# Performance work log

Hardware: AMD Instinct MI355X
Metric: run time of the kernel (lower is better)

The kernel has to match this reference:

```python
import jax, jax.numpy as jnp
import numpy as np

B, H, S, D = 2, 16, 2048, 64

def setup_inputs() -> dict:
    key = jax.random.key(0)
    kq, kk, kv, km = jax.random.split(key, 4)
    Q = jax.random.normal(kq, (B, H, S, D), dtype=jnp.float32)
    K = jax.random.normal(kk, (B, H, S, D), dtype=jnp.float32)
    V = jax.random.normal(kv, (B, H, S, D), dtype=jnp.float32)
    # padding-style boolean mask, broadcast over heads; True = masked out
    attn_mask = jax.random.randint(km, (B, 1, S, S), 0, 2).astype(jnp.bool_)
    return {"Q": Q, "K": K, "V": V, "attn_mask": attn_mask}

def reference(Q, K, V, attn_mask):
    d = Q.shape[-1]
    scale = 1.0 / np.sqrt(d).astype(np.float32)
    # [B,H,S,S] scores
    scores = jnp.einsum('bhqd,bhkd->bhqk', Q, K) * scale
    scores = jnp.where(attn_mask, jnp.float32(-1e9), scores)
    attn = jax.nn.softmax(scores, axis=-1)
    context = jnp.einsum('bhqk,bhkd->bhqd', attn, V)
    return context
```

## Files before the change

kernel.cpp:

```cpp
#include <hip/hip_runtime.h>

#define B_ 2
#define H_ 16
#define S_ 2048
#define D_ 64
#define BK 32
#define NKT (S_ / BK)
#define ZSPLIT 2
#define NKT_Z (NKT / ZSPLIT)
#define QSCALE 0.18033688011112042f
#define MFIX 16.0f

#define KSD 36
#define VTD 18
#define KS_SZ (BK * KSD)
#define VT_SZ (D_ * VTD)

#define BHSD ((size_t)B_ * H_ * S_ * D_)
#define BHS  ((size_t)B_ * H_ * S_)

typedef __attribute__((ext_vector_type(4))) float  float4v;
typedef __attribute__((ext_vector_type(2))) _Float16 half2v;
typedef __attribute__((ext_vector_type(4))) _Float16 half4v;
typedef __attribute__((ext_vector_type(8))) _Float16 half8v;
typedef __attribute__((ext_vector_type(2))) __fp16 fp16x2;
typedef __attribute__((ext_vector_type(2))) unsigned uint2v;

union H2U { half2v h; fp16x2 g; unsigned u; };
union H4U { half4v h4; half2v h2[2]; fp16x2 g2[2]; uint2v u2; };
union H8U { half8v h8; fp16x2 g2[4]; };

__device__ __forceinline__ unsigned pkh(float a, float b) {
    H2U c; c.g = __builtin_amdgcn_cvt_pkrtz(a, b);
    return c.u;
}
__device__ __forceinline__ float fexp2(float x) {
#if __has_builtin(__builtin_amdgcn_exp2f)
    return __builtin_amdgcn_exp2f(x);
#else
    return exp2f(x);
#endif
}

__device__ __forceinline__ void wg_barrier() {
    asm volatile("s_waitcnt lgkmcnt(0)\n\ts_barrier" ::: "memory");
}

struct Stage { float4 k0, k1, va, vb; };

__device__ __forceinline__ void stage_load(const float* __restrict__ Kg,
                                           const float* __restrict__ Vg,
                                           int kk, int dd, Stage& s) {
    s.k0 = *(const float4*)(Kg + (size_t)kk * D_ + dd);
    s.k1 = *(const float4*)(Kg + (size_t)(kk + 16) * D_ + dd);
    s.va = *(const float4*)(Vg + (size_t)(2 * kk) * D_ + dd);
    s.vb = *(const float4*)(Vg + (size_t)(2 * kk + 1) * D_ + dd);
}

__device__ __forceinline__ void stage_store(unsigned* KsB, unsigned* VtB,
                                            int kwa, int kwb, const int* vw,
                                            const Stage& s) {
    *(uint2v*)&KsB[kwa] = (uint2v){ pkh(s.k0.x, s.k0.y), pkh(s.k0.z, s.k0.w) };
    *(uint2v*)&KsB[kwb] = (uint2v){ pkh(s.k1.x, s.k1.y), pkh(s.k1.z, s.k1.w) };
    VtB[vw[0]] = pkh(s.va.x, s.vb.x);
    VtB[vw[1]] = pkh(s.va.y, s.vb.y);
    VtB[vw[2]] = pkh(s.va.z, s.vb.z);
    VtB[vw[3]] = pkh(s.va.w, s.vb.w);
}

__device__ __forceinline__ float4 mask2bias(int4 m) {
    float4 r;
    r.x = m.x ? -1e9f : -MFIX;  r.y = m.y ? -1e9f : -MFIX;
    r.z = m.z ? -1e9f : -MFIX;  r.w = m.w ? -1e9f : -MFIX;
    return r;
}

__global__ __launch_bounds__(256, 4)
void attn_flash_sk(const float* __restrict__ Q, const float* __restrict__ K,
                   const float* __restrict__ V, const int* __restrict__ mask,
                   float* __restrict__ Opart, float* __restrict__ Lpart)
{
    __shared__ unsigned KsAll[2 * KS_SZ];
    __shared__ unsigned VtAll[2 * VT_SZ];

    const int tid  = threadIdx.x;
    const int lane = tid & 63;
    const int l15  = lane & 15;
    const int quad = lane >> 4;
    const int wave = tid >> 6;
    const int bh   = blockIdx.y;
    const int b    = bh / H_;
    const int qbase = blockIdx.x * 64 + wave * 16;
    const size_t qkv = (size_t)bh * S_ * D_;

    const int ktBegin = blockIdx.z * NKT_Z;
    const int ktEnd   = ktBegin + NKT_Z;

    half8v qf[2];
    {
        const float* qrow = Q + qkv + (size_t)(qbase + l15) * D_ + quad * 8;
        #pragma unroll
        for (int dc = 0; dc < 2; ++dc) {
            float4 f0 = *(const float4*)(qrow + dc * 32);
            float4 f1 = *(const float4*)(qrow + dc * 32 + 4);
            H8U u;
            u.g2[0] = __builtin_amdgcn_cvt_pkrtz(f0.x * QSCALE, f0.y * QSCALE);
            u.g2[1] = __builtin_amdgcn_cvt_pkrtz(f0.z * QSCALE, f0.w * QSCALE);
            u.g2[2] = __builtin_amdgcn_cvt_pkrtz(f1.x * QSCALE, f1.y * QSCALE);
            u.g2[3] = __builtin_amdgcn_cvt_pkrtz(f1.z * QSCALE, f1.w * QSCALE);
            qf[dc] = u.h8;
        }
    }

    const int kk = tid >> 4;
    const int dd = (tid & 15) * 4;
    const int kwa = kk * KSD + (tid & 15) * 2;
    const int kwb = (kk + 16) * KSD + (tid & 15) * 2;
    int vw[4];
    #pragma unroll
    for (int m = 0; m < 4; ++m)
        vw[m] = (dd + m) * VTD + (kk ^ ((((dd + m) >> 4) & 3) << 1));

    int kroff[2][2];
    #pragma unroll
    for (int t = 0; t < 2; ++t)
        #pragma unroll
        for (int dc = 0; dc < 2; ++dc)
            kroff[t][dc] = (t * 16 + l15) * KSD + dc * 16 + quad * 4;
    int vrd[4][2];
    #pragma unroll
    for (int nb = 0; nb < 4; ++nb)
        #pragma unroll
        for (int t = 0; t < 2; ++t)
            vrd[nb][t] = (nb * 16 + l15) * VTD + ((t * 8 + quad * 2) ^ ((nb & 3) << 1));

    const int* mrow0 = mask + (size_t)b * S_ * S_ + (size_t)(qbase + l15) * S_ + quad * 4;

    float l_lane = 0.0f;
    float4v o[4];
    #pragma unroll
    for (int nb = 0; nb < 4; ++nb) o[nb] = (float4v){0.f, 0.f, 0.f, 0.f};

    const float* Kg0 = K + qkv;
    const float* Vg0 = V + qkv;

    Stage sA, sB;
    stage_load(Kg0 + (size_t)ktBegin * BK * D_, Vg0 + (size_t)ktBegin * BK * D_, kk, dd, sA);
    stage_store(KsAll, VtAll, kwa, kwb, vw, sA);
    stage_load(Kg0 + (size_t)(ktBegin + 1) * BK * D_, Vg0 + (size_t)(ktBegin + 1) * BK * D_, kk, dd, sB);
    float4 mk0 = mask2bias(*(const int4*)(mrow0 + (size_t)ktBegin * BK));
    float4 mk1 = mask2bias(*(const int4*)(mrow0 + (size_t)ktBegin * BK + 16));
    wg_barrier();

    auto iter = [&](int kt, const unsigned* KsB, const unsigned* VtB,
                    unsigned* KsN, unsigned* VtN, Stage& pre, Stage& sto) {
        const int ktn = (kt + 2 < ktEnd) ? kt + 2 : ktEnd - 1;
        stage_load(Kg0 + (size_t)ktn * BK * D_, Vg0 + (size_t)ktn * BK * D_, kk, dd, pre);
        const int mtn = (kt + 1 < ktEnd) ? kt + 1 : ktEnd - 1;
        const int* mnext = mrow0 + (size_t)mtn * BK;
        const float4 nm0 = mask2bias(*(const int4*)(mnext));
        const float4 nm1 = mask2bias(*(const int4*)(mnext + 16));

        float4v st0 = (float4v){0.f,0.f,0.f,0.f}, st1 = st0;
        {
            half8v kf;
            kf = *(const half8v*)&KsB[kroff[0][0]];
            st0 = __builtin_amdgcn_mfma_f32_16x16x32_f16(kf, qf[0], st0, 0, 0, 0);
            kf = *(const half8v*)&KsB[kroff[0][1]];
            st0 = __builtin_amdgcn_mfma_f32_16x16x32_f16(kf, qf[1], st0, 0, 0, 0);
            kf = *(const half8v*)&KsB[kroff[1][0]];
            st1 = __builtin_amdgcn_mfma_f32_16x16x32_f16(kf, qf[0], st1, 0, 0, 0);
            kf = *(const half8v*)&KsB[kroff[1][1]];
            st1 = __builtin_amdgcn_mfma_f32_16x16x32_f16(kf, qf[1], st1, 0, 0, 0);
        }

        float4v p0, p1;
        p0.x = fexp2(st0.x + mk0.x); p0.y = fexp2(st0.y + mk0.y);
        p0.z = fexp2(st0.z + mk0.z); p0.w = fexp2(st0.w + mk0.w);
        p1.x = fexp2(st1.x + mk1.x); p1.y = fexp2(st1.y + mk1.y);
        p1.z = fexp2(st1.z + mk1.z); p1.w = fexp2(st1.w + mk1.w);

        l_lane += ((p0.x + p0.y) + (p0.z + p0.w)) +
                  ((p1.x + p1.y) + (p1.z + p1.w));

        H4U pf0u, pf1u;
        pf0u.g2[0] = __builtin_amdgcn_cvt_pkrtz(p0.x, p0.y);
        pf0u.g2[1] = __builtin_amdgcn_cvt_pkrtz(p0.z, p0.w);
        pf1u.g2[0] = __builtin_amdgcn_cvt_pkrtz(p1.x, p1.y);
        pf1u.g2[1] = __builtin_amdgcn_cvt_pkrtz(p1.z, p1.w);

        #pragma unroll
        for (int nb = 0; nb < 4; ++nb) {
            H4U vf;
            vf.u2 = *(const uint2v*)&VtB[vrd[nb][0]];
            o[nb] = __builtin_amdgcn_mfma_f32_16x16x16f16(vf.h4, pf0u.h4, o[nb], 0, 0, 0);
            vf.u2 = *(const uint2v*)&VtB[vrd[nb][1]];
            o[nb] = __builtin_amdgcn_mfma_f32_16x16x16f16(vf.h4, pf1u.h4, o[nb], 0, 0, 0);
        }

        stage_store(KsN, VtN, kwa, kwb, vw, sto);
        wg_barrier();
        mk0 = nm0; mk1 = nm1;
    };

    #pragma unroll 1
    for (int kt2 = ktBegin; kt2 < ktEnd; kt2 += 2) {
        iter(kt2,     KsAll,         VtAll,         (unsigned*)KsAll + KS_SZ, (unsigned*)VtAll + VT_SZ, sA, sB);
        iter(kt2 + 1, KsAll + KS_SZ, VtAll + VT_SZ, (unsigned*)KsAll,         (unsigned*)VtAll,         sB, sA);
    }

    float ls = l_lane;
    ls += __shfl_xor(ls, 16, 64);
    ls += __shfl_xor(ls, 32, 64);

    float* orow = Opart + (size_t)blockIdx.z * BHSD + qkv
                  + (size_t)(qbase + l15) * D_ + quad * 4;
    #pragma unroll
    for (int nb = 0; nb < 4; ++nb) {
        float4 ov = { o[nb].x, o[nb].y, o[nb].z, o[nb].w };
        *(float4*)(orow + nb * 16) = ov;
    }
    if (quad == 0)
        Lpart[(size_t)blockIdx.z * BHS + (size_t)bh * S_ + qbase + l15] = ls;
}

__global__ __launch_bounds__(256)
void attn_combine(const float* __restrict__ Opart, const float* __restrict__ Lpart,
                  float* __restrict__ out)
{
    const size_t i = (size_t)blockIdx.x * 256 + threadIdx.x;
    const size_t row = i >> 4;
    const float l = Lpart[row] + Lpart[BHS + row];
    const float inv = 1.0f / l;
    const float4 a = ((const float4*)Opart)[i];
    const float4 c = ((const float4*)Opart)[BHSD / 4 + i];
    float4 r = { (a.x + c.x) * inv, (a.y + c.y) * inv,
                 (a.z + c.z) * inv, (a.w + c.w) * inv };
    ((float4*)out)[i] = r;
}

__global__ __launch_bounds__(256, 4)
void attn_flash_st(const float* __restrict__ Q, const float* __restrict__ K,
                   const float* __restrict__ V, const int* __restrict__ mask,
                   float* __restrict__ out)
{
    __shared__ unsigned KsAll[2 * KS_SZ];
    __shared__ unsigned VtAll[2 * VT_SZ];

    const int tid  = threadIdx.x;
    const int lane = tid & 63;
    const int l15  = lane & 15;
    const int quad = lane >> 4;
    const int wave = tid >> 6;
    const int bh   = blockIdx.y;
    const int b    = bh / H_;
    const int qbase = blockIdx.x * 64 + wave * 16;
    const size_t qkv = (size_t)bh * S_ * D_;

    half8v qf[2];
    {
        const float* qrow = Q + qkv + (size_t)(qbase + l15) * D_ + quad * 8;
        #pragma unroll
        for (int dc = 0; dc < 2; ++dc) {
            float4 f0 = *(const float4*)(qrow + dc * 32);
            float4 f1 = *(const float4*)(qrow + dc * 32 + 4);
            H8U u;
            u.g2[0] = __builtin_amdgcn_cvt_pkrtz(f0.x * QSCALE, f0.y * QSCALE);
            u.g2[1] = __builtin_amdgcn_cvt_pkrtz(f0.z * QSCALE, f0.w * QSCALE);
            u.g2[2] = __builtin_amdgcn_cvt_pkrtz(f1.x * QSCALE, f1.y * QSCALE);
            u.g2[3] = __builtin_amdgcn_cvt_pkrtz(f1.z * QSCALE, f1.w * QSCALE);
            qf[dc] = u.h8;
        }
    }

    const int kk = tid >> 4;
    const int dd = (tid & 15) * 4;
    const int kwa = kk * KSD + (tid & 15) * 2;
    const int kwb = (kk + 16) * KSD + (tid & 15) * 2;
    int vw[4];
    #pragma unroll
    for (int m = 0; m < 4; ++m)
        vw[m] = (dd + m) * VTD + (kk ^ ((((dd + m) >> 4) & 3) << 1));

    int kroff[2][2];
    #pragma unroll
    for (int t = 0; t < 2; ++t)
        #pragma unroll
        for (int dc = 0; dc < 2; ++dc)
            kroff[t][dc] = (t * 16 + l15) * KSD + dc * 16 + quad * 4;
    int vrd[4][2];
    #pragma unroll
    for (int nb = 0; nb < 4; ++nb)
        #pragma unroll
        for (int t = 0; t < 2; ++t)
            vrd[nb][t] = (nb * 16 + l15) * VTD + ((t * 8 + quad * 2) ^ ((nb & 3) << 1));

    const int* mrow0 = mask + (size_t)b * S_ * S_ + (size_t)(qbase + l15) * S_ + quad * 4;

    float l_lane = 0.0f;
    float4v o[4];
    #pragma unroll
    for (int nb = 0; nb < 4; ++nb) o[nb] = (float4v){0.f, 0.f, 0.f, 0.f};

    const float* Kg0 = K + qkv;
    const float* Vg0 = V + qkv;

    Stage sA, sB;
    stage_load(Kg0, Vg0, kk, dd, sA);
    stage_store(KsAll, VtAll, kwa, kwb, vw, sA);
    stage_load(Kg0 + BK * D_, Vg0 + BK * D_, kk, dd, sB);
    float4 mk0 = mask2bias(*(const int4*)(mrow0));
    float4 mk1 = mask2bias(*(const int4*)(mrow0 + 16));
    wg_barrier();

    auto iter = [&](int kt, const unsigned* KsB, const unsigned* VtB,
                    unsigned* KsN, unsigned* VtN, Stage& pre, Stage& sto) {
        const int ktn = (kt + 2 < NKT) ? kt + 2 : NKT - 1;
        stage_load(Kg0 + (size_t)ktn * BK * D_, Vg0 + (size_t)ktn * BK * D_, kk, dd, pre);
        const int mtn = (kt + 1 < NKT) ? kt + 1 : NKT - 1;
        const int* mnext = mrow0 + (size_t)mtn * BK;
        const float4 nm0 = mask2bias(*(const int4*)(mnext));
        const float4 nm1 = mask2bias(*(const int4*)(mnext + 16));

        float4v st0 = (float4v){0.f,0.f,0.f,0.f}, st1 = st0;
        {
            half8v kf;
            kf = *(const half8v*)&KsB[kroff[0][0]];
            st0 = __builtin_amdgcn_mfma_f32_16x16x32_f16(kf, qf[0], st0, 0, 0, 0);
            kf = *(const half8v*)&KsB[kroff[0][1]];
            st0 = __builtin_amdgcn_mfma_f32_16x16x32_f16(kf, qf[1], st0, 0, 0, 0);
            kf = *(const half8v*)&KsB[kroff[1][0]];
            st1 = __builtin_amdgcn_mfma_f32_16x16x32_f16(kf, qf[0], st1, 0, 0, 0);
            kf = *(const half8v*)&KsB[kroff[1][1]];
            st1 = __builtin_amdgcn_mfma_f32_16x16x32_f16(kf, qf[1], st1, 0, 0, 0);
        }

        float4v p0, p1;
        p0.x = fexp2(st0.x + mk0.x); p0.y = fexp2(st0.y + mk0.y);
        p0.z = fexp2(st0.z + mk0.z); p0.w = fexp2(st0.w + mk0.w);
        p1.x = fexp2(st1.x + mk1.x); p1.y = fexp2(st1.y + mk1.y);
        p1.z = fexp2(st1.z + mk1.z); p1.w = fexp2(st1.w + mk1.w);

        l_lane += ((p0.x + p0.y) + (p0.z + p0.w)) +
                  ((p1.x + p1.y) + (p1.z + p1.w));

        H4U pf0u, pf1u;
        pf0u.g2[0] = __builtin_amdgcn_cvt_pkrtz(p0.x, p0.y);
        pf0u.g2[1] = __builtin_amdgcn_cvt_pkrtz(p0.z, p0.w);
        pf1u.g2[0] = __builtin_amdgcn_cvt_pkrtz(p1.x, p1.y);
        pf1u.g2[1] = __builtin_amdgcn_cvt_pkrtz(p1.z, p1.w);

        #pragma unroll
        for (int nb = 0; nb < 4; ++nb) {
            H4U vf;
            vf.u2 = *(const uint2v*)&VtB[vrd[nb][0]];
            o[nb] = __builtin_amdgcn_mfma_f32_16x16x16f16(vf.h4, pf0u.h4, o[nb], 0, 0, 0);
            vf.u2 = *(const uint2v*)&VtB[vrd[nb][1]];
            o[nb] = __builtin_amdgcn_mfma_f32_16x16x16f16(vf.h4, pf1u.h4, o[nb], 0, 0, 0);
        }

        stage_store(KsN, VtN, kwa, kwb, vw, sto);
        wg_barrier();
        mk0 = nm0; mk1 = nm1;
    };

    #pragma unroll 1
    for (int kt2 = 0; kt2 < NKT; kt2 += 2) {
        iter(kt2,     KsAll,         VtAll,         (unsigned*)KsAll + KS_SZ, (unsigned*)VtAll + VT_SZ, sA, sB);
        iter(kt2 + 1, KsAll + KS_SZ, VtAll + VT_SZ, (unsigned*)KsAll,         (unsigned*)VtAll,         sB, sA);
    }

    float ls = l_lane;
    ls += __shfl_xor(ls, 16, 64);
    ls += __shfl_xor(ls, 32, 64);
    const float inv = 1.0f / ls;

    float* orow = out + qkv + (size_t)(qbase + l15) * D_ + quad * 4;
    #pragma unroll
    for (int nb = 0; nb < 4; ++nb) {
        float4 ov = { o[nb].x * inv, o[nb].y * inv, o[nb].z * inv, o[nb].w * inv };
        *(float4*)(orow + nb * 16) = ov;
    }
}

extern "C" void kernel_launch(void* const* d_in, const int* in_sizes, int n_in,
                              void* d_out, int out_size, void* d_ws, size_t ws_size,
                              hipStream_t stream) {
    const float* Q    = (const float*)d_in[0];
    const float* K    = (const float*)d_in[1];
    const float* V    = (const float*)d_in[2];
    const int*   mask = (const int*)d_in[3];
    float* out = (float*)d_out;

    const size_t opBytes = BHSD * ZSPLIT * sizeof(float);
    const size_t lpBytes = BHS  * ZSPLIT * sizeof(float);
    const size_t needFull = opBytes + lpBytes;

    if (d_ws && ws_size >= needFull) {
        float* Opart = (float*)d_ws;
        float* Lpart = (float*)((char*)d_ws + opBytes);
        attn_flash_sk<<<dim3(S_ / 64, B_ * H_, ZSPLIT), dim3(256), 0, stream>>>(
            Q, K, V, mask, Opart, Lpart);
        attn_combine<<<dim3((unsigned)(BHSD / 4 / 256)), dim3(256), 0, stream>>>(
            Opart, Lpart, out);
    } else {
        attn_flash_st<<<dim3(S_ / 64, B_ * H_), dim3(256), 0, stream>>>(
            Q, K, V, mask, out);
    }
}
```

Measured before the change: 220.2 us.

## Pre-pack K/V into fp16 LDS-image tiles via separate kernel before attention

Adds a pack_kv kernel that converts K and V to fp16 once and writes them in the exact padded and swizzled shared-memory layout, including the transposed V. The attention kernel then just copies whole tile images from global memory into LDS with vector loads, instead of each of the 32 query blocks per head redoing fp32 loads, conversion and transposed scattered stores. This removes redundant conversion work and halves K/V read bytes in the main kernel. In exchange it adds an extra launch and a global write/read of the image, and raises the occupancy hint to 6.

```diff
diff --git a/kernel.cpp b/kernel.cpp
--- a/kernel.cpp
+++ b/kernel.cpp
@@ -6,18 +6,17 @@
 #define D_ 64
 #define BK 32
 #define NKT (S_ / BK)
-#define ZSPLIT 2
-#define NKT_Z (NKT / ZSPLIT)
 #define QSCALE 0.18033688011112042f
 #define MFIX 16.0f
 
 #define KSD 36
 #define VTD 18
-#define KS_SZ (BK * KSD)
-#define VT_SZ (D_ * VTD)
+#define TILE_DW 2304
+#define TILE_BYTES 9216
 
 #define BHSD ((size_t)B_ * H_ * S_ * D_)
 #define BHS  ((size_t)B_ * H_ * S_)
+#define IMG_DW ((size_t)B_ * H_ * NKT * TILE_DW)
 
 typedef __attribute__((ext_vector_type(4))) float  float4v;
 typedef __attribute__((ext_vector_type(2))) _Float16 half2v;
@@ -25,6 +24,7 @@
 typedef __attribute__((ext_vector_type(8))) _Float16 half8v;
 typedef __attribute__((ext_vector_type(2))) __fp16 fp16x2;
 typedef __attribute__((ext_vector_type(2))) unsigned uint2v;
+typedef __attribute__((ext_vector_type(4))) unsigned uint4v;
 
 union H2U { half2v h; fp16x2 g; unsigned u; };
 union H4U { half4v h4; half2v h2[2]; fp16x2 g2[2]; uint2v u2; };
@@ -46,42 +46,49 @@
     asm volatile("s_waitcnt lgkmcnt(0)\n\ts_barrier" ::: "memory");
 }
 
-struct Stage { float4 k0, k1, va, vb; };
-
-__device__ __forceinline__ void stage_load(const float* __restrict__ Kg,
-                                           const float* __restrict__ Vg,
-                                           int kk, int dd, Stage& s) {
-    s.k0 = *(const float4*)(Kg + (size_t)kk * D_ + dd);
-    s.k1 = *(const float4*)(Kg + (size_t)(kk + 16) * D_ + dd);
-    s.va = *(const float4*)(Vg + (size_t)(2 * kk) * D_ + dd);
-    s.vb = *(const float4*)(Vg + (size_t)(2 * kk + 1) * D_ + dd);
-}
-
-__device__ __forceinline__ void stage_store(unsigned* KsB, unsigned* VtB,
-                                            int kwa, int kwb, const int* vw,
-                                            const Stage& s) {
-    *(uint2v*)&KsB[kwa] = (uint2v){ pkh(s.k0.x, s.k0.y), pkh(s.k0.z, s.k0.w) };
-    *(uint2v*)&KsB[kwb] = (uint2v){ pkh(s.k1.x, s.k1.y), pkh(s.k1.z, s.k1.w) };
-    VtB[vw[0]] = pkh(s.va.x, s.vb.x);
-    VtB[vw[1]] = pkh(s.va.y, s.vb.y);
-    VtB[vw[2]] = pkh(s.va.z, s.vb.z);
-    VtB[vw[3]] = pkh(s.va.w, s.vb.w);
-}
-
-__device__ __forceinline__ float4 mask2bias(int4 m) {
-    float4 r;
-    r.x = m.x ? -1e9f : -MFIX;  r.y = m.y ? -1e9f : -MFIX;
-    r.z = m.z ? -1e9f : -MFIX;  r.w = m.w ? -1e9f : -MFIX;
-    return r;
-}
-
-__global__ __launch_bounds__(256, 4)
-void attn_flash_sk(const float* __restrict__ Q, const float* __restrict__ K,
-                   const float* __restrict__ V, const int* __restrict__ mask,
-                   float* __restrict__ Opart, float* __restrict__ Lpart)
+__global__ __launch_bounds__(256)
+void pack_kv(const float* __restrict__ K, const float* __restrict__ V,
+             unsigned* __restrict__ img)
 {
-    __shared__ unsigned KsAll[2 * KS_SZ];
-    __shared__ unsigned VtAll[2 * VT_SZ];
+    __shared__ float Kf[32 * 64];
+    __shared__ float Vf[32 * 64];
+    const int tid = threadIdx.x;
+    const int kt = blockIdx.x, bh = blockIdx.y;
+    const size_t base = ((size_t)bh * S_ + (size_t)kt * 32) * D_;
+
+    const int rr = tid >> 4, c4 = (tid & 15) * 4;
+    *(float4*)&Kf[rr * 64 + c4]        = *(const float4*)(K + base + (size_t)rr * D_ + c4);
+    *(float4*)&Kf[(rr + 16) * 64 + c4] = *(const float4*)(K + base + (size_t)(rr + 16) * D_ + c4);
+    *(float4*)&Vf[rr * 64 + c4]        = *(const float4*)(V + base + (size_t)rr * D_ + c4);
+    *(float4*)&Vf[(rr + 16) * 64 + c4] = *(const float4*)(V + base + (size_t)(rr + 16) * D_ + c4);
+    __syncthreads();
+
+    unsigned* out = img + (size_t)(bh * NKT + kt) * TILE_DW;
+    #pragma unroll
+    for (int p = 0; p < 9; ++p) {
+        const int P = p * 256 + tid;
+        unsigned val = 0u;
+        if (P < 1152) {
+            const int r2 = P / 36, pd = P % 36;
+            if (pd < 32) val = pkh(Kf[r2 * 64 + 2 * pd], Kf[r2 * 64 + 2 * pd + 1]);
+        } else {
+            const int Pv = P - 1152;
+            const int r = Pv / 18, c = Pv % 18;
+            if (c < 16) {
+                const int ct = c ^ ((((r >> 4) & 3) << 1));
+                val = pkh(Vf[(2 * ct) * 64 + r], Vf[(2 * ct + 1) * 64 + r]);
+            }
+        }
+        out[P] = val;
+    }
+}
+
+__global__ __launch_bounds__(256, 6)
+void attn_img(const float* __restrict__ Q, const unsigned* __restrict__ img,
+              const int* __restrict__ mask, float* __restrict__ out,
+              float* __restrict__ Opart, float* __restrict__ Lpart)
+{
+    __shared__ unsigned Buf[2 * TILE_DW];
 
     const int tid  = threadIdx.x;
     const int lane = tid & 63;
@@ -93,8 +100,10 @@
     const int qbase = blockIdx.x * 64 + wave * 16;
     const size_t qkv = (size_t)bh * S_ * D_;
 
-    const int ktBegin = blockIdx.z * NKT_Z;
-    const int ktEnd   = ktBegin + NKT_Z;
+    const int zsplit = gridDim.z;
+    const int nkt    = NKT / zsplit;
+    const int ktB    = blockIdx.z * nkt;
+    const int ktE    = ktB + nkt;
 
     half8v qf[2];
     {
@@ -112,116 +121,126 @@
         }
     }
 
-    const int kk = tid >> 4;
-    const int dd = (tid & 15) * 4;
-    const int kwa = kk * KSD + (tid & 15) * 2;
-    const int kwb = (kk + 16) * KSD + (tid & 15) * 2;
-    int vw[4];
-    #pragma unroll
-    for (int m = 0; m < 4; ++m)
-        vw[m] = (dd + m) * VTD + (kk ^ ((((dd + m) >> 4) & 3) << 1));
-
-    int kroff[2][2];
-    #pragma unroll
-    for (int t = 0; t < 2; ++t)
-        #pragma unroll
-        for (int dc = 0; dc < 2; ++dc)
-            kroff[t][dc] = (t * 16 + l15) * KSD + dc * 16 + quad * 4;
-    int vrd[4][2];
+    const int kbase = l15 * KSD + quad * 4;
+    int vrd4[4];
     #pragma unroll
     for (int nb = 0; nb < 4; ++nb)
-        #pragma unroll
-        for (int t = 0; t < 2; ++t)
-            vrd[nb][t] = (nb * 16 + l15) * VTD + ((t * 8 + quad * 2) ^ ((nb & 3) << 1));
+        vrd4[nb] = 1152 + nb * 16 * VTD + l15 * VTD + ((quad * 2) ^ ((nb & 3) << 1));
 
     const int* mrow0 = mask + (size_t)b * S_ * S_ + (size_t)(qbase + l15) * S_ + quad * 4;
+
+    const unsigned* gsrc = img + (size_t)(bh * NKT + ktB) * TILE_DW;
+    const int wa = 4 * tid;
+    uint4v sa, sb; unsigned sc;
 
     float l_lane = 0.0f;
     float4v o[4];
     #pragma unroll
     for (int nb = 0; nb < 4; ++nb) o[nb] = (float4v){0.f, 0.f, 0.f, 0.f};
 
-    const float* Kg0 = K + qkv;
-    const float* Vg0 = V + qkv;
-
-    Stage sA, sB;
-    stage_load(Kg0 + (size_t)ktBegin * BK * D_, Vg0 + (size_t)ktBegin * BK * D_, kk, dd, sA);
-    stage_store(KsAll, VtAll, kwa, kwb, vw, sA);
-    stage_load(Kg0 + (size_t)(ktBegin + 1) * BK * D_, Vg0 + (size_t)(ktBegin + 1) * BK * D_, kk, dd, sB);
-    float4 mk0 = mask2bias(*(const int4*)(mrow0 + (size_t)ktBegin * BK));
-    float4 mk1 = mask2bias(*(const int4*)(mrow0 + (size_t)ktBegin * BK + 16));
+    sa = *(const uint4v*)(gsrc + wa);
+    sb = *(const uint4v*)(gsrc + 1024 + wa);
+    sc = gsrc[2048 + tid];
+    *(uint4v*)&Buf[wa]        = sa;
+    *(uint4v*)&Buf[1024 + wa] = sb;
+    Buf[2048 + tid]           = sc;
+    gsrc += TILE_DW;
+    sa = *(const uint4v*)(gsrc + wa);
+    sb = *(const uint4v*)(gsrc + 1024 + wa);
+    sc = gsrc[2048 + tid];
+    int4 mA0 = *(const int4*)(mrow0 + (size_t)ktB * BK);
+    int4 mA1 = *(const int4*)(mrow0 + (size_t)ktB * BK + 16);
+    int4 mB0, mB1;
     wg_barrier();
 
-    auto iter = [&](int kt, const unsigned* KsB, const unsigned* VtB,
-                    unsigned* KsN, unsigned* VtN, Stage& pre, Stage& sto) {
-        const int ktn = (kt + 2 < ktEnd) ? kt + 2 : ktEnd - 1;
-        stage_load(Kg0 + (size_t)ktn * BK * D_, Vg0 + (size_t)ktn * BK * D_, kk, dd, pre);
-        const int mtn = (kt + 1 < ktEnd) ? kt + 1 : ktEnd - 1;
-        const int* mnext = mrow0 + (size_t)mtn * BK;
-        const float4 nm0 = mask2bias(*(const int4*)(mnext));
-        const float4 nm1 = mask2bias(*(const int4*)(mnext + 16));
+    auto body = [&](int kt, const unsigned* cur, unsigned* oth,
+                    const int4 c0, const int4 c1, int4& n0, int4& n1) {
+        *(uint4v*)&oth[wa]        = sa;
+        *(uint4v*)&oth[1024 + wa] = sb;
+        oth[2048 + tid]           = sc;
+        if (kt + 2 < ktE) gsrc += TILE_DW;
+        sa = *(const uint4v*)(gsrc + wa);
+        sb = *(const uint4v*)(gsrc + 1024 + wa);
+        sc = gsrc[2048 + tid];
 
         float4v st0 = (float4v){0.f,0.f,0.f,0.f}, st1 = st0;
         {
             half8v kf;
-            kf = *(const half8v*)&KsB[kroff[0][0]];
+            kf = *(const half8v*)&cur[kbase];
             st0 = __builtin_amdgcn_mfma_f32_16x16x32_f16(kf, qf[0], st0, 0, 0, 0);
-            kf = *(const half8v*)&KsB[kroff[0][1]];
+            kf = *(const half8v*)&cur[kbase + 16];
             st0 = __builtin_amdgcn_mfma_f32_16x16x32_f16(kf, qf[1], st0, 0, 0, 0);
-            kf = *(const half8v*)&KsB[kroff[1][0]];
+            kf = *(const half8v*)&cur[kbase + 576];
             st1 = __builtin_amdgcn_mfma_f32_16x16x32_f16(kf, qf[0], st1, 0, 0, 0);
-            kf = *(const half8v*)&KsB[kroff[1][1]];
+            kf = *(const half8v*)&cur[kbase + 576 + 16];
             st1 = __builtin_amdgcn_mfma_f32_16x16x32_f16(kf, qf[1], st1, 0, 0, 0);
         }
 
+        const int mtn = (kt + 1 < ktE) ? kt + 1 : ktE - 1;
+        n0 = *(const int4*)(mrow0 + (size_t)mtn * BK);
+        n1 = *(const int4*)(mrow0 + (size_t)mtn * BK + 16);
+
         float4v p0, p1;
-        p0.x = fexp2(st0.x + mk0.x); p0.y = fexp2(st0.y + mk0.y);
-        p0.z = fexp2(st0.z + mk0.z); p0.w = fexp2(st0.w + mk0.w);
-        p1.x = fexp2(st1.x + mk1.x); p1.y = fexp2(st1.y + mk1.y);
-        p1.z = fexp2(st1.z + mk1.z); p1.w = fexp2(st1.w + mk1.w);
+        p0.x = fexp2(st0.x + (c0.x ? -1e9f : -MFIX));
+        p0.y = fexp2(st0.y + (c0.y ? -1e9f : -MFIX));
+        p0.z = fexp2(st0.z + (c0.z ? -1e9f : -MFIX));
+        p0.w = fexp2(st0.w + (c0.w ? -1e9f : -MFIX));
+        p1.x = fexp2(st1.x + (c1.x ? -1e9f : -MFIX));
+        p1.y = fexp2(st1.y + (c1.y ? -1e9f : -MFIX));
+        p1.z = fexp2(st1.z + (c1.z ? -1e9f : -MFIX));
+        p1.w = fexp2(st1.w + (c1.w ? -1e9f : -MFIX));
 
         l_lane += ((p0.x + p0.y) + (p0.z + p0.w)) +
                   ((p1.x + p1.y) + (p1.z + p1.w));
 
-        H4U pf0u, pf1u;
-        pf0u.g2[0] = __builtin_amdgcn_cvt_pkrtz(p0.x, p0.y);
-        pf0u.g2[1] = __builtin_amdgcn_cvt_pkrtz(p0.z, p0.w);
-        pf1u.g2[0] = __builtin_amdgcn_cvt_pkrtz(p1.x, p1.y);
-        pf1u.g2[1] = __builtin_amdgcn_cvt_pkrtz(p1.z, p1.w);
+        H4U pf0, pf1;
+        pf0.g2[0] = __builtin_amdgcn_cvt_pkrtz(p0.x, p0.y);
+        pf0.g2[1] = __builtin_amdgcn_cvt_pkrtz(p0.z, p0.w);
+        pf1.g2[0] = __builtin_amdgcn_cvt_pkrtz(p1.x, p1.y);
+        pf1.g2[1] = __builtin_amdgcn_cvt_pkrtz(p1.z, p1.w);
 
         #pragma unroll
         for (int nb = 0; nb < 4; ++nb) {
             H4U vf;
-            vf.u2 = *(const uint2v*)&VtB[vrd[nb][0]];
-            o[nb] = __builtin_amdgcn_mfma_f32_16x16x16f16(vf.h4, pf0u.h4, o[nb], 0, 0, 0);
-            vf.u2 = *(const uint2v*)&VtB[vrd[nb][1]];
-            o[nb] = __builtin_amdgcn_mfma_f32_16x16x16f16(vf.h4, pf1u.h4, o[nb], 0, 0, 0);
-        }
-
-        stage_store(KsN, VtN, kwa, kwb, vw, sto);
+            vf.u2 = *(const uint2v*)&cur[vrd4[nb]];
+            o[nb] = __builtin_amdgcn_mfma_f32_16x16x16f16(vf.h4, pf0.h4, o[nb], 0, 0, 0);
+            vf.u2 = *(const uint2v*)&cur[vrd4[nb] + 8];
+            o[nb] = __builtin_amdgcn_mfma_f32_16x16x16f16(vf.h4, pf1.h4, o[nb], 0, 0, 0);
+        }
+
         wg_barrier();
-        mk0 = nm0; mk1 = nm1;
     };
 
     #pragma unroll 1
-    for (int kt2 = ktBegin; kt2 < ktEnd; kt2 += 2) {
-        iter(kt2,     KsAll,         VtAll,         (unsigned*)KsAll + KS_SZ, (unsigned*)VtAll + VT_SZ, sA, sB);
-        iter(kt2 + 1, KsAll + KS_SZ, VtAll + VT_SZ, (unsigned*)KsAll,         (unsigned*)VtAll,         sB, sA);
+    for (int t = 0; t < nkt / 2; ++t) {
+        const int kt = ktB + 2 * t;
+        body(kt,     Buf,           Buf + TILE_DW, mA0, mA1, mB0, mB1);
+        body(kt + 1, Buf + TILE_DW, Buf,           mB0, mB1, mA0, mA1);
     }
 
     float ls = l_lane;
     ls += __shfl_xor(ls, 16, 64);
     ls += __shfl_xor(ls, 32, 64);
 
-    float* orow = Opart + (size_t)blockIdx.z * BHSD + qkv
-                  + (size_t)(qbase + l15) * D_ + quad * 4;
-    #pragma unroll
-    for (int nb = 0; nb < 4; ++nb) {
-        float4 ov = { o[nb].x, o[nb].y, o[nb].z, o[nb].w };
-        *(float4*)(orow + nb * 16) = ov;
-    }
-    if (quad == 0)
-        Lpart[(size_t)blockIdx.z * BHS + (size_t)bh * S_ + qbase + l15] = ls;
+    if (zsplit == 1) {
+        const float inv = 1.0f / ls;
+        float* orow = out + qkv + (size_t)(qbase + l15) * D_ + quad * 4;
+        #pragma unroll
+        for (int nb = 0; nb < 4; ++nb) {
+            float4 ov = { o[nb].x * inv, o[nb].y * inv, o[nb].z * inv, o[nb].w * inv };
+            *(float4*)(orow + nb * 16) = ov;
+        }
+    } else {
+        float* orow = Opart + (size_t)blockIdx.z * BHSD + qkv
+                      + (size_t)(qbase + l15) * D_ + quad * 4;
+        #pragma unroll
+        for (int nb = 0; nb < 4; ++nb) {
+            float4 ov = { o[nb].x, o[nb].y, o[nb].z, o[nb].w };
+            *(float4*)(orow + nb * 16) = ov;
+        }
+        if (quad == 0)
+            Lpart[(size_t)blockIdx.z * BHS + (size_t)bh * S_ + qbase + l15] = ls;
+    }
 }
 
 __global__ __launch_bounds__(256)
@@ -239,6 +258,38 @@
     ((float4*)out)[i] = r;
 }
 
+struct Stage { float4 k0, k1, va, vb; };
+
+__device__ __forceinline__ void stage_load(const float* __restrict__ Kg,
+                                           const float* __restrict__ Vg,
+                                           int kk, int dd, Stage& s) {
+    s.k0 = *(const float4*)(Kg + (size_t)kk * D_ + dd);
+    s.k1 = *(const float4*)(Kg + (size_t)(kk + 16) * D_ + dd);
+    s.va = *(const float4*)(Vg + (size_t)(2 * kk) * D_ + dd);
+    s.vb = *(const float4*)(Vg + (size_t)(2 * kk + 1) * D_ + dd);
+}
+
+__device__ __forceinline__ void stage_store(unsigned* KsB, unsigned* VtB,
+                                            int kwa, int kwb, const int* vw,
+                                            const Stage& s) {
+    *(uint2v*)&KsB[kwa] = (uint2v){ pkh(s.k0.x, s.k0.y), pkh(s.k0.z, s.k0.w) };
+    *(uint2v*)&KsB[kwb] = (uint2v){ pkh(s.k1.x, s.k1.y), pkh(s.k1.z, s.k1.w) };
+    VtB[vw[0]] = pkh(s.va.x, s.vb.x);
+    VtB[vw[1]] = pkh(s.va.y, s.vb.y);
+    VtB[vw[2]] = pkh(s.va.z, s.vb.z);
+    VtB[vw[3]] = pkh(s.va.w, s.vb.w);
+}
+
+__device__ __forceinline__ float4 mask2bias(int4 m) {
+    float4 r;
+    r.x = m.x ? -1e9f : -MFIX;  r.y = m.y ? -1e9f : -MFIX;
+    r.z = m.z ? -1e9f : -MFIX;  r.w = m.w ? -1e9f : -MFIX;
+    return r;
+}
+
+#define KS_SZ (BK * KSD)
+#define VT_SZ (D_ * VTD)
+
 __global__ __launch_bounds__(256, 4)
 void attn_flash_st(const float* __restrict__ Q, const float* __restrict__ K,
                    const float* __restrict__ V, const int* __restrict__ mask,
@@ -392,17 +443,24 @@
     const int*   mask = (const int*)d_in[3];
     float* out = (float*)d_out;
 
-    const size_t opBytes = BHSD * ZSPLIT * sizeof(float);
-    const size_t lpBytes = BHS  * ZSPLIT * sizeof(float);
-    const size_t needFull = opBytes + lpBytes;
-
-    if (d_ws && ws_size >= needFull) {
-        float* Opart = (float*)d_ws;
-        float* Lpart = (float*)((char*)d_ws + opBytes);
-        attn_flash_sk<<<dim3(S_ / 64, B_ * H_, ZSPLIT), dim3(256), 0, stream>>>(
-            Q, K, V, mask, Opart, Lpart);
+    const size_t imgBytes = IMG_DW * sizeof(unsigned);
+    const size_t opBytes  = BHSD * 2 * sizeof(float);
+    const size_t lpBytes  = BHS  * 2 * sizeof(float);
+
+    if (d_ws && ws_size >= imgBytes + opBytes + lpBytes) {
+        unsigned* img = (unsigned*)d_ws;
+        float* Opart = (float*)((char*)d_ws + imgBytes);
+        float* Lpart = (float*)((char*)d_ws + imgBytes + opBytes);
+        pack_kv<<<dim3(NKT, B_ * H_), dim3(256), 0, stream>>>(K, V, img);
+        attn_img<<<dim3(S_ / 64, B_ * H_, 2), dim3(256), 0, stream>>>(
+            Q, img, mask, out, Opart, Lpart);
         attn_combine<<<dim3((unsigned)(BHSD / 4 / 256)), dim3(256), 0, stream>>>(
             Opart, Lpart, out);
+    } else if (d_ws && ws_size >= imgBytes) {
+        unsigned* img = (unsigned*)d_ws;
+        pack_kv<<<dim3(NKT, B_ * H_), dim3(256), 0, stream>>>(K, V, img);
+        attn_img<<<dim3(S_ / 64, B_ * H_, 1), dim3(256), 0, stream>>>(
+            Q, img, mask, out, nullptr, nullptr);
     } else {
         attn_flash_st<<<dim3(S_ / 64, B_ * H_), dim3(256), 0, stream>>>(
             Q, K, V, mask, out);
```

Result: faster. 213.2 us (-3.2%).
